# Performance work log

Measured on AMD Instinct MI355X. Metric: run time of the kernel, lower is better.

The kernel has to match this reference:

```python
import jax, jax.numpy as jnp
import numpy as np

BATCH, SEQ, D_MODEL = 2, 4096, 1024
D_STATE, EXPAND = 64, 2
D_INNER = D_MODEL * EXPAND


def setup_inputs() -> dict:
    key = jax.random.key(0)
    ks = jax.random.split(key, 12)
    s = 0.02
    return {
        "x": jax.random.normal(ks[0], (BATCH, SEQ, D_MODEL), dtype=jnp.float32),
        "W_in": jax.random.normal(ks[1], (D_MODEL, 2 * D_INNER), dtype=jnp.float32) * s,
        "b_in": jnp.zeros((2 * D_INNER,), dtype=jnp.float32),
        "W_xp": jax.random.normal(ks[2], (D_INNER, D_STATE), dtype=jnp.float32) * s,
        "b_xp": jnp.zeros((D_STATE,), dtype=jnp.float32),
        "W_dt": jax.random.normal(ks[3], (D_INNER, D_MODEL), dtype=jnp.float32) * s,
        "b_dt": jnp.zeros((D_MODEL,), dtype=jnp.float32),
        "W_out": jax.random.normal(ks[4], (D_INNER, D_MODEL), dtype=jnp.float32) * s,
        "b_out": jnp.zeros((D_MODEL,), dtype=jnp.float32),
        "A_log": jax.random.normal(ks[5], (D_STATE,), dtype=jnp.float32),
        "D": jax.random.normal(ks[6], (D_MODEL,), dtype=jnp.float32),
    }


def _silu(v):
    return v * jax.nn.sigmoid(v)


def reference(x, W_in, b_in, W_xp, b_xp, W_dt, b_dt, W_out, b_out, A_log, D):
    # in_proj -> split into inner stream and residual gate
    xr = x @ W_in + b_in                       # [B,S,2*d_inner]
    x_inner, res = jnp.split(xr, 2, axis=-1)   # each [B,S,d_inner]
    x_inner = _silu(x_inner)

    A = -jnp.exp(A_log)                        # [N]
    delta = jax.nn.softplus(x_inner @ W_dt + b_dt)  # [B,S,d_model]
    mean_delta = delta.mean(axis=-1)           # [B,S] (scalar dt per step, as in source)
    a = jnp.exp(A[None, None, :] * mean_delta[..., None])  # [B,S,N] discrete A
    bx = x_inner @ W_xp + b_xp                 # [B,S,N] input injection

    # sequential selective-scan recurrence: state = a_t * state + bx_t
    def step(state, inp):
        a_t, bx_t = inp                        # [B,N] each
        state = a_t * state + bx_t
        return state, state.sum(axis=-1)       # emit per-batch scalar

    init = jnp.zeros((x.shape[0], D_STATE), dtype=x.dtype)
    _, s_sum = jax.lax.scan(step, init, (a.transpose(1, 0, 2), bx.transpose(1, 0, 2)))
    s_sum = s_sum.T                            # [B,S]

    y = s_sum[..., None] * x_inner             # [B,S,d_inner]
    y = y * _silu(res)
    out = y @ W_out + b_out + x * D
    return out
```

## Files before the change

kernel.cpp:

```cpp
#include <hip/hip_runtime.h>

#define SEQ 4096
#define DMODEL 1024
#define DSTATE 64
#define DINNER 2048
#define MROWS 8192
#define NCAT 1152
#define NCHUNK 64
#define LCHUNK 64

typedef __attribute__((ext_vector_type(8))) __bf16 bf16x8;
typedef __attribute__((ext_vector_type(8))) short short8;
typedef __attribute__((ext_vector_type(4))) float floatx4;

__device__ inline float bf2f(short s) {
  union { unsigned u; float f; } c;
  c.u = ((unsigned)(unsigned short)s) << 16;
  return c.f;
}
__device__ inline short f2bf(float f) {
  union { float f; unsigned u; } c; c.f = f;
  unsigned r = 0x7fffu + ((c.u >> 16) & 1u);
  return (short)((c.u + r) >> 16);
}
__device__ inline float silu_f(float v) {
  return v * __builtin_amdgcn_rcpf(1.f + __expf(-v));
}
__device__ inline float softplus_f(float v) {
  return fmaxf(v, 0.f) + log1pf(__expf(-fabsf(v)));
}
__device__ inline void gld_lds16(const void* g, void* l) {
  __builtin_amdgcn_global_load_lds(
      (__attribute__((address_space(1))) void*)g,
      (__attribute__((address_space(3))) void*)l, 16, 0, 0);
}

__device__ inline size_t permOff(int r, int k, int K) {
  return (((size_t)(r >> 4) * (K >> 3) + (k >> 3)) << 7) + ((r & 15) << 3) + (k & 7);
}

#define PP0 4096
#define PP1 (PP0 + 4096)
#define PP2 (PP1 + 2048)
#define PP3 (PP2 + 128)
#define PP4 (PP3 + 2048)

__device__ void tile_transpose_perm(const float* __restrict__ in, short* __restrict__ out,
                                    int R, int C, int bx, int by, float (*tile)[33]) {
  const int tx = threadIdx.x & 31, ty = threadIdx.x >> 5;
  const int cb = bx * 32, rb = by * 32;
#pragma unroll
  for (int i = 0; i < 32; i += 8) {
    int r = rb + ty + i, c = cb + tx;
    tile[ty + i][tx] = (r < R && c < C) ? in[(size_t)r * C + c] : 0.f;
  }
  __syncthreads();
#pragma unroll
  for (int i = 0; i < 32; i += 8) {
    int orow = cb + ty + i, oc = rb + tx;
    if (orow < C && oc < R) out[permOff(orow, oc, R)] = f2bf(tile[tx][ty + i]);
  }
}

__global__ void prepass_kernel(const float* __restrict__ x, short* __restrict__ x_bf,
                               const float* __restrict__ W_in, short* __restrict__ Wt_in,
                               const float* __restrict__ W_dt, const float* __restrict__ W_xp,
                               short* __restrict__ Bcat,
                               const float* __restrict__ W_out, short* __restrict__ Wt_out) {
  __shared__ float tile[32][33];
  const int blk = blockIdx.x;
  if (blk < PP0) {
    int o = blk * 256 + threadIdx.x;
    int m = o & 15, rest = o >> 4;
    int c = rest & 127, p = rest >> 7;
    const float* src = x + ((size_t)(p * 16 + m)) * 1024 + c * 8;
    float4 v0 = ((const float4*)src)[0];
    float4 v1 = ((const float4*)src)[1];
    short8 ov;
    ov[0] = f2bf(v0.x); ov[1] = f2bf(v0.y); ov[2] = f2bf(v0.z); ov[3] = f2bf(v0.w);
    ov[4] = f2bf(v1.x); ov[5] = f2bf(v1.y); ov[6] = f2bf(v1.z); ov[7] = f2bf(v1.w);
    ((short8*)x_bf)[o] = ov;
  } else if (blk < PP1) {
    int t = blk - PP0;
    tile_transpose_perm(W_in, Wt_in, 1024, 4096, t & 127, t >> 7, tile);
  } else if (blk < PP2) {
    int t = blk - PP1;
    tile_transpose_perm(W_dt, Bcat, 2048, 1024, t & 31, t >> 5, tile);
  } else if (blk < PP3) {
    int t = blk - PP2;
    tile_transpose_perm(W_xp, Bcat + (size_t)1024 * DINNER, 2048, 64, t & 1, t >> 1, tile);
  } else {
    int t = blk - PP3;
    tile_transpose_perm(W_out, Wt_out, 2048, 1024, t & 31, t >> 5, tile);
  }
}

template <int MODE, int KTOT, int KSL, int NB, int Z>
__global__ __launch_bounds__(256) void gemm_bt(
    const short* __restrict__ A, const short* __restrict__ Bt,
    const float* __restrict__ bias,
    void* __restrict__ out0, void* __restrict__ out1)
{
  __shared__ __attribute__((aligned(16))) short sA[128 * 32];
  __shared__ __attribute__((aligned(16))) short sB[128 * 32];

  const int tid = threadIdx.x;
  const int lane = tid & 63;
  const int w = tid >> 6;
  const int wr = w >> 1, wc = w & 1;
  const int m = lane & 15, quad = lane >> 4;

  const int xcd = blockIdx.x & 7;
  const int rest = blockIdx.x >> 3;
  constexpr int PXB = 8 * NB;
  const int z = rest / PXB;
  const int q2 = rest - z * PXB;
  const int bM = (xcd * 8 + (q2 & 7)) * 128;
  const int bN = (q2 >> 3) * 128;
  constexpr int N = NB * 128;

  floatx4 acc[4][4] = {};

  const size_t PS = (size_t)KTOT * 16;
  const short* Apan0 = A  + ((size_t)(bM >> 4) + w) * PS + lane * 8;
  const short* Apan1 = Apan0 + 4 * PS;
  const short* Bpan0 = Bt + ((size_t)(bN >> 4) + w) * PS + lane * 8;
  const short* Bpan1 = Bpan0 + 4 * PS;
  short* dA0 = sA + w * 512;
  short* dA1 = sA + (w + 4) * 512;
  short* dB0 = sB + w * 512;
  short* dB1 = sB + (w + 4) * 512;

  const int kbeg = z * KSL;
#pragma unroll 2
  for (int k0 = kbeg; k0 < kbeg + KSL; k0 += 32) {
    __syncthreads();
    const size_t ko = (size_t)k0 * 16;
    gld_lds16(Apan0 + ko, dA0);
    gld_lds16(Apan1 + ko, dA1);
    gld_lds16(Bpan0 + ko, dB0);
    gld_lds16(Bpan1 + ko, dB1);
    __syncthreads();
    bf16x8 af[4], bf[4];
#pragma unroll
    for (int rt = 0; rt < 4; ++rt)
      af[rt] = *(const bf16x8*)(sA + (((wr * 4 + rt) * 64 + quad * 16 + m) << 3));
#pragma unroll
    for (int ct = 0; ct < 4; ++ct)
      bf[ct] = *(const bf16x8*)(sB + (((wc * 4 + ct) * 64 + quad * 16 + m) << 3));
#pragma unroll
    for (int rt = 0; rt < 4; ++rt)
#pragma unroll
      for (int ct = 0; ct < 4; ++ct)
        acc[rt][ct] = __builtin_amdgcn_mfma_f32_16x16x32_bf16(af[rt], bf[ct], acc[rt][ct], 0, 0, 0);
  }

  const int rowbase = bM + wr * 64;
  const int colbase = bN + wc * 64;

  if (MODE == 0) {
    short* dst = (bN < DINNER) ? (short*)out0 : (short*)out1;
    const int cb = (bN < DINNER) ? colbase : colbase - DINNER;
#pragma unroll
    for (int rt = 0; rt < 4; ++rt) {
      const size_t rowPan = ((size_t)((rowbase >> 4) + rt)) << 8;
#pragma unroll
      for (int ct = 0; ct < 4; ++ct) {
        const int colA = colbase + ct * 16 + m;
        const int colP = cb + ct * 16 + m;
        const size_t base = ((rowPan + (colP >> 3)) << 7) + (colP & 7) + ((size_t)quad * 32);
#pragma unroll
        for (int reg = 0; reg < 4; ++reg) {
          float val = acc[rt][ct][reg] + bias[colA];
          dst[base + reg * 8] = f2bf(silu_f(val));
        }
      }
    }
  } else {
    short* dst = (short*)out0 + (size_t)z * MROWS * N;
#pragma unroll
    for (int rt = 0; rt < 4; ++rt)
#pragma unroll
      for (int ct = 0; ct < 4; ++ct) {
        const int col = colbase + ct * 16 + m;
#pragma unroll
        for (int reg = 0; reg < 4; ++reg) {
          const int r = rowbase + rt * 16 + quad * 4 + reg;
          dst[(size_t)r * N + col] = f2bf(acc[rt][ct][reg]);
        }
      }
  }
}

__global__ void g2_epilogue(const short* __restrict__ p, const float* __restrict__ b_dt,
                            const float* __restrict__ b_xp,
                            float* __restrict__ md_sum, float* __restrict__ bx) {
  const int r = blockIdx.x, t = threadIdx.x;
  const size_t base0 = (size_t)r * NCAT;
  const size_t base1 = base0 + (size_t)MROWS * NCAT;
  float s = 0.f;
#pragma unroll
  for (int j = 0; j < 4; ++j) {
    const int c = t + j * 256;
    float v = bf2f(p[base0 + c]) + bf2f(p[base1 + c]) + b_dt[c];
    s += softplus_f(v);
  }
  s += __shfl_xor(s, 1);  s += __shfl_xor(s, 2);  s += __shfl_xor(s, 4);
  s += __shfl_xor(s, 8);  s += __shfl_xor(s, 16); s += __shfl_xor(s, 32);
  __shared__ float wsum[4];
  if ((t & 63) == 0) wsum[t >> 6] = s;
  __syncthreads();
  if (t == 0) md_sum[r] = wsum[0] + wsum[1] + wsum[2] + wsum[3];
  if (t < 64)
    bx[(size_t)r * DSTATE + t] =
        bf2f(p[base0 + 1024 + t]) + bf2f(p[base1 + 1024 + t]) + b_xp[t];
}

__global__ void g4_epilogue(const short* __restrict__ p, const float* __restrict__ b_out,
                            const float* __restrict__ x, const float* __restrict__ Dv,
                            float* __restrict__ out) {
  const int r = blockIdx.x, c = threadIdx.x * 4;
  const size_t o = (size_t)r * DMODEL + c;
  short4 a0 = *(const short4*)(p + o);
  short4 a1 = *(const short4*)(p + (size_t)MROWS * DMODEL + o);
  float4 xv = *(const float4*)(x + o);
  float4 ov;
  ov.x = bf2f(a0.x) + bf2f(a1.x) + b_out[c + 0] + xv.x * Dv[c + 0];
  ov.y = bf2f(a0.y) + bf2f(a1.y) + b_out[c + 1] + xv.y * Dv[c + 1];
  ov.z = bf2f(a0.z) + bf2f(a1.z) + b_out[c + 2] + xv.z * Dv[c + 2];
  ov.w = bf2f(a0.w) + bf2f(a1.w) + b_out[c + 3] + xv.w * Dv[c + 3];
  *(float4*)(out + o) = ov;
}

__global__ void scan_phase1(const float* __restrict__ md_sum, const float* __restrict__ A_log,
                            const float* __restrict__ bx,
                            float* __restrict__ chunk_prod, float* __restrict__ chunk_end) {
  const int n = threadIdx.x;
  const int c = blockIdx.x & (NCHUNK - 1);
  const int b = blockIdx.x >> 6;
  const float An = -__expf(A_log[n]);
  float prod = 1.f, st = 0.f;
  const int t0 = c * LCHUNK;
  for (int i = 0; i < LCHUNK; ++i) {
    const int t = t0 + i;
    const float md = md_sum[b * SEQ + t] * (1.f / DMODEL);
    const float a = __expf(An * md);
    st = a * st + bx[((size_t)(b * SEQ + t)) * DSTATE + n];
    prod *= a;
  }
  chunk_prod[(b * NCHUNK + c) * DSTATE + n] = prod;
  chunk_end [(b * NCHUNK + c) * DSTATE + n] = st;
}

__global__ void scan_phase3(const float* __restrict__ md_sum, const float* __restrict__ A_log,
                            const float* __restrict__ bx,
                            const float* __restrict__ chunk_prod,
                            const float* __restrict__ chunk_end,
                            float* __restrict__ s_sum) {
  const int n = threadIdx.x;
  const int c = blockIdx.x & (NCHUNK - 1);
  const int b = blockIdx.x >> 6;
  const float An = -__expf(A_log[n]);
  float st = 0.f;
  for (int cc = 0; cc < c; ++cc) {
    const size_t idx = ((size_t)(b * NCHUNK + cc)) * DSTATE + n;
    st = chunk_prod[idx] * st + chunk_end[idx];
  }
  const int t0 = c * LCHUNK;
  for (int i = 0; i < LCHUNK; ++i) {
    const int t = t0 + i;
    const float md = md_sum[b * SEQ + t] * (1.f / DMODEL);
    const float a = __expf(An * md);
    st = a * st + bx[((size_t)(b * SEQ + t)) * DSTATE + n];
    float v = st;
    v += __shfl_xor(v, 32); v += __shfl_xor(v, 16); v += __shfl_xor(v, 8);
    v += __shfl_xor(v, 4);  v += __shfl_xor(v, 2);  v += __shfl_xor(v, 1);
    if (n == 0) s_sum[b * SEQ + t] = v;
  }
}

__global__ void ymul_kernel(const short* __restrict__ xi, const short* __restrict__ g,
                            const float* __restrict__ s_sum, short* __restrict__ y) {
  const int o = blockIdx.x * 256 + threadIdx.x;
  const int row = ((o >> 12) << 4) | (o & 15);
  const size_t base = (size_t)o * 8;
  const float s = s_sum[row];
  short8 xv = *(const short8*)(xi + base);
  short8 gv = *(const short8*)(g + base);
  short8 yv;
#pragma unroll
  for (int k = 0; k < 8; ++k) yv[k] = f2bf(s * bf2f(xv[k]) * bf2f(gv[k]));
  *(short8*)(y + base) = yv;
}

extern "C" void kernel_launch(void* const* d_in, const int* in_sizes, int n_in,
                              void* d_out, int out_size, void* d_ws, size_t ws_size,
                              hipStream_t stream) {
  const float* x     = (const float*)d_in[0];
  const float* W_in  = (const float*)d_in[1];
  const float* b_in  = (const float*)d_in[2];
  const float* W_xp  = (const float*)d_in[3];
  const float* b_xp  = (const float*)d_in[4];
  const float* W_dt  = (const float*)d_in[5];
  const float* b_dt  = (const float*)d_in[6];
  const float* W_out = (const float*)d_in[7];
  const float* b_out = (const float*)d_in[8];
  const float* A_log = (const float*)d_in[9];
  const float* Dv    = (const float*)d_in[10];

  char* ws = (char*)d_ws;
  size_t off = 0;
  auto alloc = [&](size_t bytes) -> void* {
    void* p = (void*)(ws + off);
    off += (bytes + 255) & ~(size_t)255;
    return p;
  };
  short* x_bf    = (short*)alloc((size_t)MROWS * DMODEL * 2);
  short* Wt_in   = (short*)alloc((size_t)4096 * 1024 * 2);
  short* Bcat    = (short*)alloc((size_t)NCAT * DINNER * 2);
  short* Wt_out  = (short*)alloc((size_t)1024 * 2048 * 2);
  short* xi      = (short*)alloc((size_t)MROWS * DINNER * 2);
  short* gbuf    = (short*)alloc((size_t)MROWS * DINNER * 2);
  short* ybuf    = (short*)alloc((size_t)MROWS * DINNER * 2);
  short* p2      = (short*)alloc((size_t)2 * MROWS * NCAT * 2);
  float* md_sum  = (float*)alloc((size_t)MROWS * 4);
  float* bx      = (float*)alloc((size_t)MROWS * DSTATE * 4);
  float* cprod   = (float*)alloc((size_t)2 * NCHUNK * DSTATE * 4);
  float* cend    = (float*)alloc((size_t)2 * NCHUNK * DSTATE * 4);
  float* s_sum   = (float*)alloc((size_t)MROWS * 4);

  prepass_kernel<<<PP4, 256, 0, stream>>>(x, x_bf, W_in, Wt_in, W_dt, W_xp, Bcat, W_out, Wt_out);

  gemm_bt<0, 1024, 1024, 32, 1><<<2048, 256, 0, stream>>>(x_bf, Wt_in, b_in, xi, gbuf);
  gemm_bt<1, 2048, 1024, 9, 2><<<1152, 256, 0, stream>>>(xi, Bcat, nullptr, p2, nullptr);
  g2_epilogue<<<MROWS, 256, 0, stream>>>(p2, b_dt, b_xp, md_sum, bx);
  scan_phase1<<<2 * NCHUNK, DSTATE, 0, stream>>>(md_sum, A_log, bx, cprod, cend);
  scan_phase3<<<2 * NCHUNK, DSTATE, 0, stream>>>(md_sum, A_log, bx, cprod, cend, s_sum);
  ymul_kernel<<<MROWS * DINNER / 8 / 256, 256, 0, stream>>>(xi, gbuf, s_sum, ybuf);
  gemm_bt<1, 2048, 1024, 8, 2><<<1024, 256, 0, stream>>>(ybuf, Wt_out, nullptr, xi, nullptr);
  g4_epilogue<<<MROWS, 256, 0, stream>>>(xi, b_out, x, Dv, (float*)d_out);
}
```

Before: 418.3 us.

## Fuse GEMM epilogues into atomic split-K accumulation and merge softplus into scan phase

Removes the g2 and g4 epilogue kernels. The last GEMM now atomically adds fp32 partials into an output that the prepass seeds with b_out + x*D. The W_xp columns of the middle GEMM are atomically added into bx, which the prepass seeds with b_xp. The softplus mean reduction moves into a new fused scan phase-1 kernel that stages chunk data in LDS. This saves launches and the bf16 partial round-trips, but adds atomic traffic, and the order of the fp32 additions becomes nondeterministic.

After: 489.8 us. 17.1% more time.

```diff
diff --git a/kernel.cpp b/kernel.cpp
--- a/kernel.cpp
+++ b/kernel.cpp
@@ -5,7 +5,6 @@
 #define DSTATE 64
 #define DINNER 2048
 #define MROWS 8192
-#define NCAT 1152
 #define NCHUNK 64
 #define LCHUNK 64
 
@@ -44,6 +43,8 @@
 #define PP2 (PP1 + 2048)
 #define PP3 (PP2 + 128)
 #define PP4 (PP3 + 2048)
+#define PP5 (PP4 + 512)
+#define PP6 (PP5 + 8192)
 
 __device__ void tile_transpose_perm(const float* __restrict__ in, short* __restrict__ out,
                                     int R, int C, int bx, int by, float (*tile)[33]) {
@@ -66,7 +67,10 @@
                                const float* __restrict__ W_in, short* __restrict__ Wt_in,
                                const float* __restrict__ W_dt, const float* __restrict__ W_xp,
                                short* __restrict__ Bcat,
-                               const float* __restrict__ W_out, short* __restrict__ Wt_out) {
+                               const float* __restrict__ W_out, short* __restrict__ Wt_out,
+                               const float* __restrict__ b_xp, float* __restrict__ bx,
+                               const float* __restrict__ b_out, const float* __restrict__ Dv,
+                               float* __restrict__ dout) {
   __shared__ float tile[32][33];
   const int blk = blockIdx.x;
   if (blk < PP0) {
@@ -89,9 +93,24 @@
   } else if (blk < PP3) {
     int t = blk - PP2;
     tile_transpose_perm(W_xp, Bcat + (size_t)1024 * DINNER, 2048, 64, t & 1, t >> 1, tile);
-  } else {
+  } else if (blk < PP4) {
     int t = blk - PP3;
     tile_transpose_perm(W_out, Wt_out, 2048, 1024, t & 31, t >> 5, tile);
+  } else if (blk < PP5) {
+    int idx = (blk - PP4) * 256 + threadIdx.x;
+    int n = (idx & 15) * 4;
+    float4 bv = { b_xp[n], b_xp[n + 1], b_xp[n + 2], b_xp[n + 3] };
+    ((float4*)bx)[idx] = bv;
+  } else {
+    int idx = (blk - PP5) * 256 + threadIdx.x;
+    int c = (idx & 255) * 4;
+    float4 xv = ((const float4*)x)[idx];
+    float4 ov;
+    ov.x = b_out[c + 0] + xv.x * Dv[c + 0];
+    ov.y = b_out[c + 1] + xv.y * Dv[c + 1];
+    ov.z = b_out[c + 2] + xv.z * Dv[c + 2];
+    ov.w = b_out[c + 3] + xv.w * Dv[c + 3];
+    ((float4*)dout)[idx] = ov;
   }
 }
 
@@ -117,7 +136,6 @@
   const int q2 = rest - z * PXB;
   const int bM = (xcd * 8 + (q2 & 7)) * 128;
   const int bN = (q2 >> 3) * 128;
-  constexpr int N = NB * 128;
 
   floatx4 acc[4][4] = {};
 
@@ -176,8 +194,36 @@
         }
       }
     }
+  } else if (MODE == 1) {
+    if (bN < 1024) {
+      short* dst = (short*)out0 + (size_t)z * MROWS * 1024;
+#pragma unroll
+      for (int rt = 0; rt < 4; ++rt)
+#pragma unroll
+        for (int ct = 0; ct < 4; ++ct) {
+          const int col = colbase + ct * 16 + m;
+#pragma unroll
+          for (int reg = 0; reg < 4; ++reg) {
+            const int r = rowbase + rt * 16 + quad * 4 + reg;
+            dst[(size_t)r * 1024 + col] = f2bf(acc[rt][ct][reg]);
+          }
+        }
+    } else if (wc == 0) {
+      float* bxp = (float*)out1;
+#pragma unroll
+      for (int rt = 0; rt < 4; ++rt)
+#pragma unroll
+        for (int ct = 0; ct < 4; ++ct) {
+          const int cr = ct * 16 + m;
+#pragma unroll
+          for (int reg = 0; reg < 4; ++reg) {
+            const int r = rowbase + rt * 16 + quad * 4 + reg;
+            atomicAdd(&bxp[(size_t)r * DSTATE + cr], acc[rt][ct][reg]);
+          }
+        }
+    }
   } else {
-    short* dst = (short*)out0 + (size_t)z * MROWS * N;
+    float* dst = (float*)out0;
 #pragma unroll
     for (int rt = 0; rt < 4; ++rt)
 #pragma unroll
@@ -186,70 +232,60 @@
 #pragma unroll
         for (int reg = 0; reg < 4; ++reg) {
           const int r = rowbase + rt * 16 + quad * 4 + reg;
-          dst[(size_t)r * N + col] = f2bf(acc[rt][ct][reg]);
+          atomicAdd(&dst[(size_t)r * 1024 + col], acc[rt][ct][reg]);
         }
       }
   }
 }
 
-__global__ void g2_epilogue(const short* __restrict__ p, const float* __restrict__ b_dt,
-                            const float* __restrict__ b_xp,
-                            float* __restrict__ md_sum, float* __restrict__ bx) {
-  const int r = blockIdx.x, t = threadIdx.x;
-  const size_t base0 = (size_t)r * NCAT;
-  const size_t base1 = base0 + (size_t)MROWS * NCAT;
-  float s = 0.f;
-#pragma unroll
-  for (int j = 0; j < 4; ++j) {
-    const int c = t + j * 256;
-    float v = bf2f(p[base0 + c]) + bf2f(p[base1 + c]) + b_dt[c];
-    s += softplus_f(v);
-  }
-  s += __shfl_xor(s, 1);  s += __shfl_xor(s, 2);  s += __shfl_xor(s, 4);
-  s += __shfl_xor(s, 8);  s += __shfl_xor(s, 16); s += __shfl_xor(s, 32);
-  __shared__ float wsum[4];
-  if ((t & 63) == 0) wsum[t >> 6] = s;
-  __syncthreads();
-  if (t == 0) md_sum[r] = wsum[0] + wsum[1] + wsum[2] + wsum[3];
-  if (t < 64)
-    bx[(size_t)r * DSTATE + t] =
-        bf2f(p[base0 + 1024 + t]) + bf2f(p[base1 + 1024 + t]) + b_xp[t];
-}
-
-__global__ void g4_epilogue(const short* __restrict__ p, const float* __restrict__ b_out,
-                            const float* __restrict__ x, const float* __restrict__ Dv,
-                            float* __restrict__ out) {
-  const int r = blockIdx.x, c = threadIdx.x * 4;
-  const size_t o = (size_t)r * DMODEL + c;
-  short4 a0 = *(const short4*)(p + o);
-  short4 a1 = *(const short4*)(p + (size_t)MROWS * DMODEL + o);
-  float4 xv = *(const float4*)(x + o);
-  float4 ov;
-  ov.x = bf2f(a0.x) + bf2f(a1.x) + b_out[c + 0] + xv.x * Dv[c + 0];
-  ov.y = bf2f(a0.y) + bf2f(a1.y) + b_out[c + 1] + xv.y * Dv[c + 1];
-  ov.z = bf2f(a0.z) + bf2f(a1.z) + b_out[c + 2] + xv.z * Dv[c + 2];
-  ov.w = bf2f(a0.w) + bf2f(a1.w) + b_out[c + 3] + xv.w * Dv[c + 3];
-  *(float4*)(out + o) = ov;
-}
-
-__global__ void scan_phase1(const float* __restrict__ md_sum, const float* __restrict__ A_log,
-                            const float* __restrict__ bx,
-                            float* __restrict__ chunk_prod, float* __restrict__ chunk_end) {
-  const int n = threadIdx.x;
+__global__ __launch_bounds__(256) void scan1_fused(
+    const short* __restrict__ p2, const float* __restrict__ b_dt,
+    const float* __restrict__ A_log, const float* __restrict__ bx,
+    float* __restrict__ md_sum, float* __restrict__ chunk_prod,
+    float* __restrict__ chunk_end) {
   const int c = blockIdx.x & (NCHUNK - 1);
   const int b = blockIdx.x >> 6;
-  const float An = -__expf(A_log[n]);
-  float prod = 1.f, st = 0.f;
-  const int t0 = c * LCHUNK;
-  for (int i = 0; i < LCHUNK; ++i) {
-    const int t = t0 + i;
-    const float md = md_sum[b * SEQ + t] * (1.f / DMODEL);
-    const float a = __expf(An * md);
-    st = a * st + bx[((size_t)(b * SEQ + t)) * DSTATE + n];
-    prod *= a;
-  }
-  chunk_prod[(b * NCHUNK + c) * DSTATE + n] = prod;
-  chunk_end [(b * NCHUNK + c) * DSTATE + n] = st;
+  const int tid = threadIdx.x, w = tid >> 6, lane = tid & 63;
+  __shared__ float mdL[64];
+  __shared__ float bxL[64 * 64];
+
+  const int r0 = b * SEQ + c * LCHUNK;
+  const float4* bxg = (const float4*)(bx + (size_t)r0 * DSTATE);
+  float4* bxl4 = (float4*)bxL;
+  for (int i = tid; i < 1024; i += 256) bxl4[i] = bxg[i];
+  float bd[16];
+#pragma unroll
+  for (int j = 0; j < 16; ++j) bd[j] = b_dt[lane * 16 + j];
+  for (int j = 0; j < 16; ++j) {
+    const int i = w * 16 + j;
+    const size_t base0 = (size_t)(r0 + i) * 1024 + lane * 16;
+    const size_t base1 = base0 + (size_t)MROWS * 1024;
+    short8 a0 = *(const short8*)(p2 + base0);
+    short8 a1 = *(const short8*)(p2 + base0 + 8);
+    short8 c0 = *(const short8*)(p2 + base1);
+    short8 c1 = *(const short8*)(p2 + base1 + 8);
+    float s = 0.f;
+#pragma unroll
+    for (int k = 0; k < 8; ++k) {
+      s += softplus_f(bf2f(a0[k]) + bf2f(c0[k]) + bd[k]);
+      s += softplus_f(bf2f(a1[k]) + bf2f(c1[k]) + bd[8 + k]);
+    }
+    s += __shfl_xor(s, 1);  s += __shfl_xor(s, 2);  s += __shfl_xor(s, 4);
+    s += __shfl_xor(s, 8);  s += __shfl_xor(s, 16); s += __shfl_xor(s, 32);
+    if (lane == 0) { mdL[i] = s; md_sum[r0 + i] = s; }
+  }
+  __syncthreads();
+  if (w == 0) {
+    const float An = -__expf(A_log[lane]);
+    float prod = 1.f, st = 0.f;
+    for (int i = 0; i < LCHUNK; ++i) {
+      const float a = __expf(An * (mdL[i] * (1.f / DMODEL)));
+      st = a * st + bxL[i * 64 + lane];
+      prod *= a;
+    }
+    chunk_prod[(b * NCHUNK + c) * DSTATE + lane] = prod;
+    chunk_end [(b * NCHUNK + c) * DSTATE + lane] = st;
+  }
 }
 
 __global__ void scan_phase3(const float* __restrict__ md_sum, const float* __restrict__ A_log,
@@ -267,6 +303,7 @@
     st = chunk_prod[idx] * st + chunk_end[idx];
   }
   const int t0 = c * LCHUNK;
+#pragma unroll 4
   for (int i = 0; i < LCHUNK; ++i) {
     const int t = t0 + i;
     const float md = md_sum[b * SEQ + t] * (1.f / DMODEL);
@@ -317,26 +354,26 @@
   };
   short* x_bf    = (short*)alloc((size_t)MROWS * DMODEL * 2);
   short* Wt_in   = (short*)alloc((size_t)4096 * 1024 * 2);
-  short* Bcat    = (short*)alloc((size_t)NCAT * DINNER * 2);
+  short* Bcat    = (short*)alloc((size_t)1152 * DINNER * 2);
   short* Wt_out  = (short*)alloc((size_t)1024 * 2048 * 2);
   short* xi      = (short*)alloc((size_t)MROWS * DINNER * 2);
   short* gbuf    = (short*)alloc((size_t)MROWS * DINNER * 2);
   short* ybuf    = (short*)alloc((size_t)MROWS * DINNER * 2);
-  short* p2      = (short*)alloc((size_t)2 * MROWS * NCAT * 2);
+  short* p2      = (short*)alloc((size_t)2 * MROWS * 1024 * 2);
   float* md_sum  = (float*)alloc((size_t)MROWS * 4);
   float* bx      = (float*)alloc((size_t)MROWS * DSTATE * 4);
   float* cprod   = (float*)alloc((size_t)2 * NCHUNK * DSTATE * 4);
   float* cend    = (float*)alloc((size_t)2 * NCHUNK * DSTATE * 4);
   float* s_sum   = (float*)alloc((size_t)MROWS * 4);
 
-  prepass_kernel<<<PP4, 256, 0, stream>>>(x, x_bf, W_in, Wt_in, W_dt, W_xp, Bcat, W_out, Wt_out);
+  prepass_kernel<<<PP6, 256, 0, stream>>>(x, x_bf, W_in, Wt_in, W_dt, W_xp, Bcat,
+                                          W_out, Wt_out, b_xp, bx, b_out, Dv,
+                                          (float*)d_out);
 
   gemm_bt<0, 1024, 1024, 32, 1><<<2048, 256, 0, stream>>>(x_bf, Wt_in, b_in, xi, gbuf);
-  gemm_bt<1, 2048, 1024, 9, 2><<<1152, 256, 0, stream>>>(xi, Bcat, nullptr, p2, nullptr);
-  g2_epilogue<<<MROWS, 256, 0, stream>>>(p2, b_dt, b_xp, md_sum, bx);
-  scan_phase1<<<2 * NCHUNK, DSTATE, 0, stream>>>(md_sum, A_log, bx, cprod, cend);
+  gemm_bt<1, 2048, 1024, 9, 2><<<1152, 256, 0, stream>>>(xi, Bcat, nullptr, p2, bx);
+  scan1_fused<<<2 * NCHUNK, 256, 0, stream>>>(p2, b_dt, A_log, bx, md_sum, cprod, cend);
   scan_phase3<<<2 * NCHUNK, DSTATE, 0, stream>>>(md_sum, A_log, bx, cprod, cend, s_sum);
   ymul_kernel<<<MROWS * DINNER / 8 / 256, 256, 0, stream>>>(xi, gbuf, s_sum, ybuf);
-  gemm_bt<1, 2048, 1024, 8, 2><<<1024, 256, 0, stream>>>(ybuf, Wt_out, nullptr, xi, nullptr);
-  g4_epilogue<<<MROWS, 256, 0, stream>>>(xi, b_out, x, Dv, (float*)d_out);
-}
+  gemm_bt<2, 2048, 1024, 8, 2><<<1024, 256, 0, stream>>>(ybuf, Wt_out, nullptr, d_out, nullptr);
+}
```
